# Kernel tuning notes

Measured on AMD Instinct MI355X. Metric: run time of the kernel, lower is better.

## Reference

```python
import jax, jax.numpy as jnp
import numpy as np

NBITS = 8
MAXQ = float(2**NBITS - 1)  # 255 for uint8 asymmetric quantization


def asym_quantize(x):
    """Per-tensor asymmetric quantization to the [0, 255] grid.

    x ~ scale * (q - zero), with scale = (max-min)/255, zero = round(-min/scale).
    Returns (q, scale, zero) with q kept in float32 holding integer values.
    """
    xmax = jnp.max(x)
    xmin = jnp.min(x)
    scale = (xmax - xmin) / MAXQ
    zero = jnp.round(-xmin / scale)
    q = jnp.clip(jnp.round(x / scale) + zero, 0.0, MAXQ)
    return q, scale, zero


def setup_inputs() -> dict:
    key = jax.random.key(0)
    kA, kB = jax.random.split(key)
    A = jax.random.normal(kA, (4096, 2048), dtype=jnp.float32)
    B = jax.random.normal(kB, (2048, 4096), dtype=jnp.float32)
    return {"A": A, "B": B}


def reference(A, B):
    # Quantize both operands per-tensor asymmetrically.
    qA, sA, zA = asym_quantize(A)  # [M, K]
    qB, sB, zB = asym_quantize(B)  # [K, N]
    K = A.shape[1]

    # Integer GEMM on the quantized values (exact int accumulation in int32).
    acc = jnp.matmul(qA.astype(jnp.int32), qB.astype(jnp.int32)).astype(jnp.float32)  # [M, N]

    # Fused asymmetric dequant epilogue:
    # A @ B = sA*sB * (qA@qB - zA * colsum(qB) - zB * rowsum(qA) + K*zA*zB)
    rowsum_qA = jnp.sum(qA, axis=1, keepdims=True)   # [M, 1]
    colsum_qB = jnp.sum(qB, axis=0, keepdims=True)   # [1, N]
    out = (sA * sB) * (acc - zA * colsum_qB - zB * rowsum_qA
                       + jnp.float32(K) * zA * zB)
    return out
```

## Files before the change

kernel.cpp:

```cpp
#include <hip/hip_runtime.h>
#include <math.h>


#define M_DIM 4096
#define K_DIM 2048
#define N_DIM 4096

using int4v = __attribute__((ext_vector_type(4))) int;

typedef __attribute__((address_space(1))) const void glb_cv;
typedef __attribute__((address_space(3))) void lds_v;

__device__ __forceinline__ int qbyte(float x, float s, float z) {
    float q = fminf(fmaxf(rintf(x / s) + z, 0.0f), 255.0f);
    return (int)q - 128;
}

__device__ __forceinline__ int sum4(int w) {
    return (int)(signed char)(w) + (int)(signed char)(w >> 8) +
           (int)(signed char)(w >> 16) + (int)(signed char)(w >> 24);
}

__global__ void minmax_stage1(const float* __restrict__ A,
                              const float* __restrict__ B,
                              float* __restrict__ partials) {
    int b = blockIdx.x;
    const float* src = (b < 512) ? A : B;
    int lb = (b < 512) ? b : b - 512;
    const float4* v = (const float4*)src + (long)lb * 4096;
    float mn = INFINITY, mx = -INFINITY;
    for (int i = threadIdx.x; i < 4096; i += 256) {
        float4 x = v[i];
        mn = fminf(mn, fminf(fminf(x.x, x.y), fminf(x.z, x.w)));
        mx = fmaxf(mx, fmaxf(fmaxf(x.x, x.y), fmaxf(x.z, x.w)));
    }
    for (int off = 32; off; off >>= 1) {
        mn = fminf(mn, __shfl_down(mn, off));
        mx = fmaxf(mx, __shfl_down(mx, off));
    }
    __shared__ float smn[4], smx[4];
    int w = threadIdx.x >> 6;
    if ((threadIdx.x & 63) == 0) { smn[w] = mn; smx[w] = mx; }
    __syncthreads();
    if (threadIdx.x == 0) {
        mn = fminf(fminf(smn[0], smn[1]), fminf(smn[2], smn[3]));
        mx = fmaxf(fmaxf(smx[0], smx[1]), fmaxf(smx[2], smx[3]));
        partials[2 * b] = mn;
        partials[2 * b + 1] = mx;
    }
}

__global__ void minmax_stage2(const float* __restrict__ partials,
                              float* __restrict__ qp) {
    int t = threadIdx.x;
    float mnA = INFINITY, mxA = -INFINITY, mnB = INFINITY, mxB = -INFINITY;
    for (int i = t; i < 512; i += 256) {
        mnA = fminf(mnA, partials[2 * i]);
        mxA = fmaxf(mxA, partials[2 * i + 1]);
        mnB = fminf(mnB, partials[2 * (i + 512)]);
        mxB = fmaxf(mxB, partials[2 * (i + 512) + 1]);
    }
    for (int off = 32; off; off >>= 1) {
        mnA = fminf(mnA, __shfl_down(mnA, off));
        mxA = fmaxf(mxA, __shfl_down(mxA, off));
        mnB = fminf(mnB, __shfl_down(mnB, off));
        mxB = fmaxf(mxB, __shfl_down(mxB, off));
    }
    __shared__ float s[4][4];
    int w = t >> 6;
    if ((t & 63) == 0) { s[w][0] = mnA; s[w][1] = mxA; s[w][2] = mnB; s[w][3] = mxB; }
    __syncthreads();
    if (t == 0) {
        for (int i = 1; i < 4; i++) {
            mnA = fminf(mnA, s[i][0]); mxA = fmaxf(mxA, s[i][1]);
            mnB = fminf(mnB, s[i][2]); mxB = fmaxf(mxB, s[i][3]);
        }
        float sA = (mxA - mnA) / 255.0f;
        float zA = rintf(-mnA / sA);
        float sB = (mxB - mnB) / 255.0f;
        float zB = rintf(-mnB / sB);
        qp[0] = sA; qp[1] = zA; qp[2] = sB; qp[3] = zB;
    }
}

__global__ void quantA_kernel(const float* __restrict__ X,
                              signed char* __restrict__ Q,
                              const float* __restrict__ qp) {
    float s = qp[0], z = qp[1];
    long base = ((long)blockIdx.x * 256 + threadIdx.x) * 16;
    const float4* v = (const float4*)(X + base);
    union { signed char c[16]; int4 i4; } u;
#pragma unroll
    for (int j = 0; j < 4; j++) {
        float4 x = v[j];
        u.c[j * 4 + 0] = (signed char)qbyte(x.x, s, z);
        u.c[j * 4 + 1] = (signed char)qbyte(x.y, s, z);
        u.c[j * 4 + 2] = (signed char)qbyte(x.z, s, z);
        u.c[j * 4 + 3] = (signed char)qbyte(x.w, s, z);
    }
    *(int4*)(Q + base) = u.i4;
}

__global__ void quantBT_kernel(const float* __restrict__ B,
                               signed char* __restrict__ BT,
                               const float* __restrict__ qp) {
    __shared__ __align__(16) signed char tile[64][80];
    float s = qp[2], z = qp[3];
    int k0 = blockIdx.x * 64, n0 = blockIdx.y * 64;
    int t = threadIdx.x;
    int cn = (t & 15) * 4;
    int rk = t >> 4;
#pragma unroll
    for (int rr = 0; rr < 64; rr += 16) {
        int k = rk + rr;
        float4 x = *(const float4*)&B[(long)(k0 + k) * N_DIM + n0 + cn];
        tile[cn + 0][k] = (signed char)qbyte(x.x, s, z);
        tile[cn + 1][k] = (signed char)qbyte(x.y, s, z);
        tile[cn + 2][k] = (signed char)qbyte(x.z, s, z);
        tile[cn + 3][k] = (signed char)qbyte(x.w, s, z);
    }
    __syncthreads();
    int n2 = t >> 2, kc = (t & 3) * 16;
    *(int4*)&BT[(long)(n0 + n2) * K_DIM + k0 + kc] = *(const int4*)&tile[n2][kc];
}

__global__ void sums_kernel(const signed char* __restrict__ A8,
                            const signed char* __restrict__ B8T,
                            int* __restrict__ rowA, int* __restrict__ colB) {
    int row = blockIdx.x * 4 + (threadIdx.x >> 6);
    int lane = threadIdx.x & 63;
    const signed char* src = (row < 4096) ? A8 : B8T;
    int* dst = (row < 4096) ? rowA : colB;
    int r = (row < 4096) ? row : row - 4096;
    const int4* p = (const int4*)(src + (long)r * K_DIM);
    int acc = 0;
#pragma unroll
    for (int i = 0; i < 2; i++) {
        int4 w = p[lane + i * 64];
        acc += sum4(w.x) + sum4(w.y) + sum4(w.z) + sum4(w.w);
    }
    for (int off = 32; off; off >>= 1) acc += __shfl_down(acc, off);
    if (lane == 0) dst[r] = acc;
}

__global__ void gemm_i8(const signed char* __restrict__ A8,
                        const signed char* __restrict__ B8T,
                        const int* __restrict__ rowA,
                        const int* __restrict__ colB,
                        const float* __restrict__ qp,
                        float* __restrict__ out) {
    __shared__ __align__(16) signed char As[128 * 64];
    __shared__ __align__(16) signed char Bs[128 * 64];

    int r0 = blockIdx.y * 128;
    int c0 = blockIdx.x * 128;
    int t = threadIdx.x, lane = t & 63, wave = t >> 6;

    int4v acc[4][4];
#pragma unroll
    for (int i = 0; i < 4; i++)
#pragma unroll
        for (int j = 0; j < 4; j++) acc[i][j] = (int4v){0, 0, 0, 0};

    int wm = (wave >> 1) * 64;
    int wn = (wave & 1) * 64;
    int ca0 = wave * 128 + lane;

    int kg = (lane >> 4) * 16;
    int mrow = lane & 15;

    for (int k0 = 0; k0 < K_DIM; k0 += 64) {
        __syncthreads();
#pragma unroll
        for (int j = 0; j < 2; j++) {
            int ch = ca0 + j * 64;
            const signed char* ga = A8 + (long)(r0 + (ch >> 2)) * K_DIM + k0 + (ch & 3) * 16;
            __builtin_amdgcn_global_load_lds((glb_cv*)ga, (lds_v*)(As + ch * 16), 16, 0, 0);
            const signed char* gb = B8T + (long)(c0 + (ch >> 2)) * K_DIM + k0 + (ch & 3) * 16;
            __builtin_amdgcn_global_load_lds((glb_cv*)gb, (lds_v*)(Bs + ch * 16), 16, 0, 0);
        }
        __syncthreads();

        int4v af[4], bf[4];
#pragma unroll
        for (int i = 0; i < 4; i++)
            af[i] = *(const int4v*)&As[(wm + i * 16 + mrow) * 64 + kg];
#pragma unroll
        for (int j = 0; j < 4; j++)
            bf[j] = *(const int4v*)&Bs[(wn + j * 16 + mrow) * 64 + kg];
#pragma unroll
        for (int i = 0; i < 4; i++)
#pragma unroll
            for (int j = 0; j < 4; j++)
                acc[i][j] = __builtin_amdgcn_mfma_i32_16x16x64_i8(af[i], bf[j], acc[i][j], 0, 0, 0);
    }

    float sA = qp[0], zA = qp[1], sB = qp[2], zB = qp[3];
    int cA = 128 - (int)zA, cB = 128 - (int)zB;
    float ss = sA * sB;
    int Kzz = K_DIM * cA * cB;
    int colb = c0 + wn + (lane & 15);
    int rquad = (lane >> 4) * 4;
#pragma unroll
    for (int i = 0; i < 4; i++) {
#pragma unroll
        for (int j = 0; j < 4; j++) {
            int cc = colb + j * 16;
            int cbn = colB[cc];
#pragma unroll
            for (int r = 0; r < 4; r++) {
                int rr = r0 + wm + i * 16 + rquad + r;
                int v = acc[i][j][r] + cB * rowA[rr] + cA * cbn + Kzz;
                out[(long)rr * N_DIM + cc] = ss * (float)v;
            }
        }
    }
}

extern "C" void kernel_launch(void* const* d_in, const int* in_sizes, int n_in,
                              void* d_out, int out_size, void* d_ws, size_t ws_size,
                              hipStream_t stream) {
    const float* A = (const float*)d_in[0];
    const float* B = (const float*)d_in[1];
    float* out = (float*)d_out;
    char* ws = (char*)d_ws;

    signed char* A8  = (signed char*)ws;
    signed char* B8T = (signed char*)(ws + 8388608);
    int*   rowA      = (int*)(ws + 16777216);
    int*   colB      = (int*)(ws + 16793600);
    float* partials  = (float*)(ws + 16809984);
    float* qp        = (float*)(ws + 16818176);

    minmax_stage1<<<1024, 256, 0, stream>>>(A, B, partials);
    minmax_stage2<<<1, 256, 0, stream>>>(partials, qp);
    quantA_kernel<<<2048, 256, 0, stream>>>(A, A8, qp);
    quantBT_kernel<<<dim3(32, 64), 256, 0, stream>>>(B, B8T, qp);
    sums_kernel<<<2048, 256, 0, stream>>>(A8, B8T, rowA, colB);
    gemm_i8<<<dim3(32, 32), 256, 0, stream>>>(A8, B8T, rowA, colB, qp, out);
}
```

Measured before the change: 171.8 us.

## Fuse row/col sums into quant kernels, enlarge GEMM tile, swizzle LDS

Removes the separate sums kernel by computing A row sums inside the quantization kernel through a block reduction, and B column sums in the transpose-quantize kernel through atomics into a buffer zeroed in the stage-2 reduction. The GEMM block tile grows from 128x128 to 256x128, so each wave holds twice as many accumulators, and it gets launch bounds for two blocks per CU. An XOR swizzle on the 16-byte k-chunks is meant to reduce LDS bank conflicts on fragment reads. The epilogue hoists the row-sum terms out of the inner loop. This trades extra register pressure and atomic traffic for fewer launches and more data reuse per LDS load.

```diff
diff --git a/kernel.cpp b/kernel.cpp
--- a/kernel.cpp
+++ b/kernel.cpp
@@ -51,8 +51,10 @@
 }
 
 __global__ void minmax_stage2(const float* __restrict__ partials,
-                              float* __restrict__ qp) {
+                              float* __restrict__ qp,
+                              int* __restrict__ colB) {
     int t = threadIdx.x;
+    for (int i = t; i < N_DIM; i += 256) colB[i] = 0;
     float mnA = INFINITY, mxA = -INFINITY, mnB = INFINITY, mxB = -INFINITY;
     for (int i = t; i < 512; i += 256) {
         mnA = fminf(mnA, partials[2 * i]);
@@ -85,25 +87,38 @@
 
 __global__ void quantA_kernel(const float* __restrict__ X,
                               signed char* __restrict__ Q,
-                              const float* __restrict__ qp) {
+                              const float* __restrict__ qp,
+                              int* __restrict__ rowA) {
     float s = qp[0], z = qp[1];
-    long base = ((long)blockIdx.x * 256 + threadIdx.x) * 16;
+    int t = threadIdx.x;
+    long base = (long)blockIdx.x * 4096 + (long)t * 16;
     const float4* v = (const float4*)(X + base);
     union { signed char c[16]; int4 i4; } u;
+    int ls = 0;
 #pragma unroll
     for (int j = 0; j < 4; j++) {
         float4 x = v[j];
-        u.c[j * 4 + 0] = (signed char)qbyte(x.x, s, z);
-        u.c[j * 4 + 1] = (signed char)qbyte(x.y, s, z);
-        u.c[j * 4 + 2] = (signed char)qbyte(x.z, s, z);
-        u.c[j * 4 + 3] = (signed char)qbyte(x.w, s, z);
+        int q0 = qbyte(x.x, s, z), q1 = qbyte(x.y, s, z);
+        int q2 = qbyte(x.z, s, z), q3 = qbyte(x.w, s, z);
+        u.c[j * 4 + 0] = (signed char)q0;
+        u.c[j * 4 + 1] = (signed char)q1;
+        u.c[j * 4 + 2] = (signed char)q2;
+        u.c[j * 4 + 3] = (signed char)q3;
+        ls += q0 + q1 + q2 + q3;
     }
     *(int4*)(Q + base) = u.i4;
+    for (int off = 32; off; off >>= 1) ls += __shfl_down(ls, off);
+    __shared__ int ws[4];
+    if ((t & 63) == 0) ws[t >> 6] = ls;
+    __syncthreads();
+    if (t == 0) rowA[blockIdx.x * 2] = ws[0] + ws[1];
+    if (t == 128) rowA[blockIdx.x * 2 + 1] = ws[2] + ws[3];
 }
 
 __global__ void quantBT_kernel(const float* __restrict__ B,
                                signed char* __restrict__ BT,
-                               const float* __restrict__ qp) {
+                               const float* __restrict__ qp,
+                               int* __restrict__ colB) {
     __shared__ __align__(16) signed char tile[64][80];
     float s = qp[2], z = qp[3];
     int k0 = blockIdx.x * 64, n0 = blockIdx.y * 64;
@@ -121,75 +136,77 @@
     }
     __syncthreads();
     int n2 = t >> 2, kc = (t & 3) * 16;
-    *(int4*)&BT[(long)(n0 + n2) * K_DIM + k0 + kc] = *(const int4*)&tile[n2][kc];
-}
-
-__global__ void sums_kernel(const signed char* __restrict__ A8,
-                            const signed char* __restrict__ B8T,
-                            int* __restrict__ rowA, int* __restrict__ colB) {
-    int row = blockIdx.x * 4 + (threadIdx.x >> 6);
-    int lane = threadIdx.x & 63;
-    const signed char* src = (row < 4096) ? A8 : B8T;
-    int* dst = (row < 4096) ? rowA : colB;
-    int r = (row < 4096) ? row : row - 4096;
-    const int4* p = (const int4*)(src + (long)r * K_DIM);
-    int acc = 0;
-#pragma unroll
-    for (int i = 0; i < 2; i++) {
-        int4 w = p[lane + i * 64];
-        acc += sum4(w.x) + sum4(w.y) + sum4(w.z) + sum4(w.w);
-    }
-    for (int off = 32; off; off >>= 1) acc += __shfl_down(acc, off);
-    if (lane == 0) dst[r] = acc;
-}
-
-__global__ void gemm_i8(const signed char* __restrict__ A8,
-                        const signed char* __restrict__ B8T,
-                        const int* __restrict__ rowA,
-                        const int* __restrict__ colB,
-                        const float* __restrict__ qp,
-                        float* __restrict__ out) {
-    __shared__ __align__(16) signed char As[128 * 64];
+    int4 w = *(const int4*)&tile[n2][kc];
+    *(int4*)&BT[(long)(n0 + n2) * K_DIM + k0 + kc] = w;
+    int ls = sum4(w.x) + sum4(w.y) + sum4(w.z) + sum4(w.w);
+    ls += __shfl_down(ls, 2);
+    ls += __shfl_down(ls, 1);
+    if ((t & 3) == 0) atomicAdd(&colB[n0 + n2], ls);
+}
+
+__global__ __launch_bounds__(256, 2) void gemm_i8(
+        const signed char* __restrict__ A8,
+        const signed char* __restrict__ B8T,
+        const int* __restrict__ rowA,
+        const int* __restrict__ colB,
+        const float* __restrict__ qp,
+        float* __restrict__ out) {
+    __shared__ __align__(16) signed char As[256 * 64];
     __shared__ __align__(16) signed char Bs[128 * 64];
 
-    int r0 = blockIdx.y * 128;
+    int r0 = blockIdx.y * 256;
     int c0 = blockIdx.x * 128;
     int t = threadIdx.x, lane = t & 63, wave = t >> 6;
 
-    int4v acc[4][4];
-#pragma unroll
-    for (int i = 0; i < 4; i++)
+    int4v acc[8][4];
+#pragma unroll
+    for (int i = 0; i < 8; i++)
 #pragma unroll
         for (int j = 0; j < 4; j++) acc[i][j] = (int4v){0, 0, 0, 0};
 
-    int wm = (wave >> 1) * 64;
+    int wm = (wave >> 1) * 128;
     int wn = (wave & 1) * 64;
-    int ca0 = wave * 128 + lane;
-
-    int kg = (lane >> 4) * 16;
     int mrow = lane & 15;
+    int g = lane >> 4;
+    int kq = ((g ^ ((mrow >> 1) & 3)) * 16);
+
+    long aoff[4], boff[2];
+#pragma unroll
+    for (int j = 0; j < 4; j++) {
+        int ch = t + 256 * j;
+        int row = ch >> 2, c = ch & 3;
+        int gk = c ^ ((row >> 1) & 3);
+        aoff[j] = (long)(r0 + row) * K_DIM + gk * 16;
+    }
+#pragma unroll
+    for (int j = 0; j < 2; j++) {
+        int ch = t + 256 * j;
+        int row = ch >> 2, c = ch & 3;
+        int gk = c ^ ((row >> 1) & 3);
+        boff[j] = (long)(c0 + row) * K_DIM + gk * 16;
+    }
 
     for (int k0 = 0; k0 < K_DIM; k0 += 64) {
         __syncthreads();
 #pragma unroll
-        for (int j = 0; j < 2; j++) {
-            int ch = ca0 + j * 64;
-            const signed char* ga = A8 + (long)(r0 + (ch >> 2)) * K_DIM + k0 + (ch & 3) * 16;
-            __builtin_amdgcn_global_load_lds((glb_cv*)ga, (lds_v*)(As + ch * 16), 16, 0, 0);
-            const signed char* gb = B8T + (long)(c0 + (ch >> 2)) * K_DIM + k0 + (ch & 3) * 16;
-            __builtin_amdgcn_global_load_lds((glb_cv*)gb, (lds_v*)(Bs + ch * 16), 16, 0, 0);
-        }
+        for (int j = 0; j < 4; j++)
+            __builtin_amdgcn_global_load_lds((glb_cv*)(A8 + aoff[j] + k0),
+                                             (lds_v*)(As + (t + 256 * j) * 16), 16, 0, 0);
+#pragma unroll
+        for (int j = 0; j < 2; j++)
+            __builtin_amdgcn_global_load_lds((glb_cv*)(B8T + boff[j] + k0),
+                                             (lds_v*)(Bs + (t + 256 * j) * 16), 16, 0, 0);
         __syncthreads();
 
-        int4v af[4], bf[4];
-#pragma unroll
-        for (int i = 0; i < 4; i++)
-            af[i] = *(const int4v*)&As[(wm + i * 16 + mrow) * 64 + kg];
+        int4v af[8], bf[4];
+#pragma unroll
+        for (int i = 0; i < 8; i++)
+            af[i] = *(const int4v*)&As[(wm + i * 16 + mrow) * 64 + kq];
 #pragma unroll
         for (int j = 0; j < 4; j++)
-            bf[j] = *(const int4v*)&Bs[(wn + j * 16 + mrow) * 64 + kg];
-#pragma unroll
-        for (int i = 0; i < 4; i++)
+            bf[j] = *(const int4v*)&Bs[(wn + j * 16 + mrow) * 64 + kq];
+#pragma unroll
+        for (int i = 0; i < 8; i++)
 #pragma unroll
             for (int j = 0; j < 4; j++)
                 acc[i][j] = __builtin_amdgcn_mfma_i32_16x16x64_i8(af[i], bf[j], acc[i][j], 0, 0, 0);
@@ -199,19 +216,21 @@
     int cA = 128 - (int)zA, cB = 128 - (int)zB;
     float ss = sA * sB;
     int Kzz = K_DIM * cA * cB;
-    int colb = c0 + wn + (lane & 15);
-    int rquad = (lane >> 4) * 4;
-#pragma unroll
-    for (int i = 0; i < 4; i++) {
+    int ocol = c0 + wn + mrow;
+    int orow = r0 + wm + g * 4;
+#pragma unroll
+    for (int i = 0; i < 8; i++) {
+        int ra[4];
+#pragma unroll
+        for (int r = 0; r < 4; r++) ra[r] = cB * rowA[orow + i * 16 + r] + Kzz;
 #pragma unroll
         for (int j = 0; j < 4; j++) {
-            int cc = colb + j * 16;
-            int cbn = colB[cc];
+            int cc = ocol + j * 16;
+            int can = cA * colB[cc];
 #pragma unroll
             for (int r = 0; r < 4; r++) {
-                int rr = r0 + wm + i * 16 + rquad + r;
-                int v = acc[i][j][r] + cB * rowA[rr] + cA * cbn + Kzz;
-                out[(long)rr * N_DIM + cc] = ss * (float)v;
+                int v = acc[i][j][r] + ra[r] + can;
+                out[(long)(orow + i * 16 + r) * N_DIM + cc] = ss * (float)v;
             }
         }
     }
@@ -233,9 +252,8 @@
     float* qp        = (float*)(ws + 16818176);
 
     minmax_stage1<<<1024, 256, 0, stream>>>(A, B, partials);
-    minmax_stage2<<<1, 256, 0, stream>>>(partials, qp);
-    quantA_kernel<<<2048, 256, 0, stream>>>(A, A8, qp);
-    quantBT_kernel<<<dim3(32, 64), 256, 0, stream>>>(B, B8T, qp);
-    sums_kernel<<<2048, 256, 0, stream>>>(A8, B8T, rowA, colB);
-    gemm_i8<<<dim3(32, 32), 256, 0, stream>>>(A8, B8T, rowA, colB, qp, out);
-}
+    minmax_stage2<<<1, 256, 0, stream>>>(partials, qp, colB);
+    quantA_kernel<<<2048, 256, 0, stream>>>(A, A8, qp, rowA);
+    quantBT_kernel<<<dim3(32, 64), 256, 0, stream>>>(B, B8T, qp, colB);
+    gemm_i8<<<dim3(32, 16), 256, 0, stream>>>(A8, B8T, rowA, colB, qp, out);
+}
```

After: 170.0 us. No clear change (-1.0%).
